# Optimization experiments

Hardware: AMD Instinct MI355X
Metric: run time of the kernel (lower is better)

## Reference

```python
import jax, jax.numpy as jnp
import numpy as np

N, E, F, H, C, ED = 10000, 160000, 4, 32, 4, 2  # nodes, edges, in_feat, hidden, classes, edge_dim


def _init(key, shape, fan_in):
    return jax.random.normal(key, shape, jnp.float32) / np.float32(np.sqrt(fan_in))


def setup_inputs() -> dict:
    key = jax.random.key(0)
    ks = iter(jax.random.split(key, 40))
    inp = {
        "x": jax.random.normal(next(ks), (N, F), jnp.float32),
        "edge_index": jax.random.randint(next(ks), (2, E), 0, N, dtype=jnp.int32),
        "edge_attr": jax.random.normal(next(ks), (E, ED), jnp.float32),
    }
    for i, din in enumerate([F, H, H]):
        inp[f"w1_{i}"] = _init(next(ks), (ED, H), ED)
        inp[f"b1_{i}"] = jnp.zeros((H,), jnp.float32)
        inp[f"w2_{i}"] = _init(next(ks), (H, din * H), H)
        inp[f"b2_{i}"] = jnp.zeros((din * H,), jnp.float32)
        inp[f"root_{i}"] = _init(next(ks), (din, H), din)
        inp[f"bias_{i}"] = jnp.zeros((H,), jnp.float32)
    inp["fc_w"] = _init(next(ks), (H, C), H)
    inp["fc_b"] = jnp.zeros((C,), jnp.float32)
    return inp


def _nnconv(x, src, dst, edge_attr, w1, b1, w2, b2, root, bias):
    # edge MLP -> per-edge weight matrix [E, din, H]
    h = jax.nn.relu(edge_attr @ w1 + b1)                      # [E, H]
    W = (h @ w2 + b2).reshape(E, x.shape[1], -1)              # [E, din, H]
    msg = jnp.einsum('ei,eio->eo', x[src], W)                 # gather + per-edge matvec
    agg = jax.ops.segment_sum(msg, dst, num_segments=N)       # scatter-add to targets
    return agg + x @ root + bias                              # root weight + bias (NNConv)


def reference(x, edge_index, edge_attr,
              w1_0, b1_0, w2_0, b2_0, root_0, bias_0,
              w1_1, b1_1, w2_1, b2_1, root_1, bias_1,
              w1_2, b1_2, w2_2, b2_2, root_2, bias_2,
              fc_w, fc_b):
    src, dst = edge_index[0], edge_index[1]
    layers = [(w1_0, b1_0, w2_0, b2_0, root_0, bias_0),
              (w1_1, b1_1, w2_1, b2_1, root_1, bias_1),
              (w1_2, b1_2, w2_2, b2_2, root_2, bias_2)]
    for p in layers:
        x = jax.nn.relu(_nnconv(x, src, dst, edge_attr, *p))  # dropout=0 -> no-op
    logits = x @ fc_w + fc_b
    return jax.nn.log_softmax(logits, axis=1)
```

## Files before the change

### kernel.cpp

```cpp
#include <hip/hip_runtime.h>
#include <hip/hip_bf16.h>
#include <math.h>

#define N_NODES 10000
#define N_EDGES 160000

typedef __attribute__((ext_vector_type(8))) short bf16x8;
typedef __attribute__((ext_vector_type(4))) float f32x4;

static __device__ inline unsigned short f2b(float v) {
    __hip_bfloat16 b = __float2bfloat16(v);
    return *reinterpret_cast<unsigned short*>(&b);
}

__global__ __launch_bounds__(256) void k_tw2z(const float* __restrict__ s0,
                                              const float* __restrict__ s1,
                                              const float* __restrict__ s2,
                                              float* __restrict__ t0,
                                              float* __restrict__ t1,
                                              float* __restrict__ t2,
                                              int* __restrict__ cnt) {
    int tid = blockIdx.x * 256 + threadIdx.x;
    if (tid < 10240) { cnt[tid] = 0; return; }
    int d = tid - 10240;
    if (d < 4096) {
        int i = d >> 10, j = d & 1023, o = j >> 5, k = j & 31;
        t0[d] = s0[k * 128 + i * 32 + o];
    } else if (d < 4096 + 32768) {
        int q = d - 4096;
        int i = q >> 10, j = q & 1023, o = j >> 5, k = j & 31;
        t1[q] = s1[k * 1024 + i * 32 + o];
    } else if (d < 4096 + 65536) {
        int q = d - 4096 - 32768;
        int i = q >> 10, j = q & 1023, o = j >> 5, k = j & 31;
        t2[q] = s2[k * 1024 + i * 32 + o];
    }
}

__global__ __launch_bounds__(256) void k_hist(const int* __restrict__ ei,
                                              int* __restrict__ cnt) {
    int e = blockIdx.x * 256 + threadIdx.x;
    if (e < N_EDGES) atomicAdd(&cnt[ei[e]], 1);
}

__global__ __launch_bounds__(256) void k_scan(const int* __restrict__ cnt,
                                              int* __restrict__ off,
                                              int* __restrict__ cursor) {
    __shared__ int part[256];
    int t = threadIdx.x;
    int base = t * 40;
    int s = 0;
    for (int i = 0; i < 40; ++i) {
        int idx = base + i;
        if (idx < N_NODES) s += cnt[idx];
    }
    part[t] = s;
    __syncthreads();
    for (int d = 1; d < 256; d <<= 1) {
        int v = (t >= d) ? part[t - d] : 0;
        __syncthreads();
        part[t] += v;
        __syncthreads();
    }
    int run = part[t] - s;
    for (int i = 0; i < 40; ++i) {
        int idx = base + i;
        if (idx < N_NODES) {
            off[idx] = run;
            cursor[idx] = run;
            run += cnt[idx];
        }
    }
    if (t == 255) off[N_NODES] = run;
}

__global__ __launch_bounds__(256) void k_scatter_h(const int* __restrict__ ei,
                                                   const float* __restrict__ ea,
                                                   int* __restrict__ cursor,
                                                   int* __restrict__ dst_s,
                                                   const float* __restrict__ w1a, const float* __restrict__ b1a,
                                                   const float* __restrict__ w1b, const float* __restrict__ b1b,
                                                   const float* __restrict__ w1c, const float* __restrict__ b1c,
                                                   unsigned short* __restrict__ h0,
                                                   unsigned short* __restrict__ h1,
                                                   unsigned short* __restrict__ h2) {
    int e = blockIdx.x * 256 + threadIdx.x;
    if (e >= N_EDGES) return;
    float a0 = ea[2 * e], a1 = ea[2 * e + 1];
    int src = ei[e], dst = ei[N_EDGES + e];
    int pos = atomicAdd(&cursor[src], 1);
    dst_s[pos] = dst;
    const float* W1[3] = {w1a, w1b, w1c};
    const float* B1[3] = {b1a, b1b, b1c};
    unsigned short* H[3] = {h0, h1, h2};
#pragma unroll
    for (int l = 0; l < 3; ++l) {
        unsigned int pk[16];
#pragma unroll
        for (int j = 0; j < 16; ++j) {
            float v0 = fmaxf(a0 * W1[l][2 * j]     + a1 * W1[l][32 + 2 * j]     + B1[l][2 * j],     0.f);
            float v1 = fmaxf(a0 * W1[l][2 * j + 1] + a1 * W1[l][32 + 2 * j + 1] + B1[l][2 * j + 1], 0.f);
            pk[j] = (unsigned int)f2b(v0) | ((unsigned int)f2b(v1) << 16);
        }
        uint4* dp = (uint4*)(H[l] + (size_t)pos * 32);
        dp[0] = make_uint4(pk[0], pk[1], pk[2], pk[3]);
        dp[1] = make_uint4(pk[4], pk[5], pk[6], pk[7]);
        dp[2] = make_uint4(pk[8], pk[9], pk[10], pk[11]);
        dp[3] = make_uint4(pk[12], pk[13], pk[14], pk[15]);
    }
}

template <int DIN, bool FIRST>
__global__ __launch_bounds__(256) void k_G(const float* __restrict__ xin,
                                           const float* __restrict__ w2t,
                                           const float* __restrict__ b2,
                                           const float* __restrict__ root,
                                           const float* __restrict__ bias,
                                           unsigned short* __restrict__ Gb,
                                           float* __restrict__ xb2,
                                           float* __restrict__ agg) {
    const int t = threadIdx.x;
    const int n0 = blockIdx.x * 16;

    __shared__ float xs[16 * DIN];
    for (int idx = t; idx < 16 * DIN; idx += 256) {
        int m = idx / DIN, i = idx - m * DIN;
        float v = xin[(size_t)(n0 + m) * DIN + i];
        if (!FIRST) v = v > 0.f ? v : 0.f;
        xs[idx] = v;
    }
    __syncthreads();

    float acc[16][4];
#pragma unroll
    for (int m = 0; m < 16; ++m)
        acc[m][0] = acc[m][1] = acc[m][2] = acc[m][3] = 0.f;

#pragma unroll
    for (int i = 0; i < DIN; ++i) {
        const float4 w = *(const float4*)(w2t + i * 1024 + t * 4);
#pragma unroll
        for (int m = 0; m < 16; ++m) {
            float xv = xs[m * DIN + i];
            acc[m][0] += xv * w.x;
            acc[m][1] += xv * w.y;
            acc[m][2] += xv * w.z;
            acc[m][3] += xv * w.w;
        }
    }
#pragma unroll
    for (int m = 0; m < 16; ++m) {
        unsigned int p0 = (unsigned int)f2b(acc[m][0]) | ((unsigned int)f2b(acc[m][1]) << 16);
        unsigned int p1 = (unsigned int)f2b(acc[m][2]) | ((unsigned int)f2b(acc[m][3]) << 16);
        *(uint2*)(Gb + (size_t)(n0 + m) * 1024 + t * 4) = make_uint2(p0, p1);
    }

    for (int idx = t; idx < 512; idx += 256) {
        int m = idx >> 5, o = idx & 31;
        float ab = 0.f, ar = bias[o];
#pragma unroll
        for (int i = 0; i < DIN; ++i) {
            float xv = xs[m * DIN + i];
            ab += xv * b2[i * 32 + o];
            ar += xv * root[i * 32 + o];
        }
        size_t p = (size_t)(n0 + m) * 32 + o;
        xb2[p] = ab;
        agg[p] = ar;
    }
}

__global__ __launch_bounds__(256) void k_edge(const int* __restrict__ off,
                                              const int* __restrict__ dst_s,
                                              const unsigned short* __restrict__ hb,
                                              const unsigned short* __restrict__ Gb,
                                              const float* __restrict__ xb2,
                                              float* __restrict__ agg) {
    int t = threadIdx.x;
    int lane = t & 63;
    int n = blockIdx.x * 4 + (t >> 6);
    int col = lane & 15;
    int quad = lane >> 4;

    const bf16x8 b_lo = *(const bf16x8*)(Gb + (size_t)n * 1024 + col * 32 + quad * 8);
    const bf16x8 b_hi = *(const bf16x8*)(Gb + (size_t)n * 1024 + (col + 16) * 32 + quad * 8);
    float xb_lo = xb2[(size_t)n * 32 + col];
    float xb_hi = xb2[(size_t)n * 32 + 16 + col];

    int jb = off[n], je = off[n + 1];
    for (int e0 = jb; e0 < je; e0 += 16) {
        int eA = e0 + col;
        bf16x8 afrag = {0, 0, 0, 0, 0, 0, 0, 0};
        if (eA < je) afrag = *(const bf16x8*)(hb + (size_t)eA * 32 + quad * 8);
        f32x4 acc_lo = {xb_lo, xb_lo, xb_lo, xb_lo};
        f32x4 acc_hi = {xb_hi, xb_hi, xb_hi, xb_hi};
        acc_lo = __builtin_amdgcn_mfma_f32_16x16x32_bf16(afrag, b_lo, acc_lo, 0, 0, 0);
        acc_hi = __builtin_amdgcn_mfma_f32_16x16x32_bf16(afrag, b_hi, acc_hi, 0, 0, 0);
#pragma unroll
        for (int r = 0; r < 4; ++r) {
            int er = e0 + quad * 4 + r;
            if (er < je) {
                int d = dst_s[er];
                atomicAdd(&agg[(size_t)d * 32 + col], acc_lo[r]);
                atomicAdd(&agg[(size_t)d * 32 + 16 + col], acc_hi[r]);
            }
        }
    }
}

__global__ __launch_bounds__(64) void k_final(const float* __restrict__ agg,
                                              const float* __restrict__ fcw,
                                              const float* __restrict__ fcb,
                                              float* __restrict__ out) {
    int n = blockIdx.x * 64 + threadIdx.x;
    if (n >= N_NODES) return;
    float l0 = fcb[0], l1 = fcb[1], l2 = fcb[2], l3 = fcb[3];
#pragma unroll
    for (int o = 0; o < 32; ++o) {
        float xv = agg[(size_t)n * 32 + o];
        xv = xv > 0.f ? xv : 0.f;
        l0 += xv * fcw[o * 4 + 0];
        l1 += xv * fcw[o * 4 + 1];
        l2 += xv * fcw[o * 4 + 2];
        l3 += xv * fcw[o * 4 + 3];
    }
    float m = fmaxf(fmaxf(l0, l1), fmaxf(l2, l3));
    float s = expf(l0 - m) + expf(l1 - m) + expf(l2 - m) + expf(l3 - m);
    float lse = m + logf(s);
    out[(size_t)n * 4 + 0] = l0 - lse;
    out[(size_t)n * 4 + 1] = l1 - lse;
    out[(size_t)n * 4 + 2] = l2 - lse;
    out[(size_t)n * 4 + 3] = l3 - lse;
}

extern "C" void kernel_launch(void* const* d_in, const int* in_sizes, int n_in,
                              void* d_out, int out_size, void* d_ws, size_t ws_size,
                              hipStream_t stream) {
    const float* x0 = (const float*)d_in[0];
    const int*   ei = (const int*)d_in[1];
    const float* ea = (const float*)d_in[2];
    const float *W1[3], *B1[3], *W2[3], *B2[3], *RT[3], *BS[3];
    for (int l = 0; l < 3; ++l) {
        W1[l] = (const float*)d_in[3 + 6 * l];
        B1[l] = (const float*)d_in[4 + 6 * l];
        W2[l] = (const float*)d_in[5 + 6 * l];
        B2[l] = (const float*)d_in[6 + 6 * l];
        RT[l] = (const float*)d_in[7 + 6 * l];
        BS[l] = (const float*)d_in[8 + 6 * l];
    }
    const float* fcw = (const float*)d_in[21];
    const float* fcb = (const float*)d_in[22];
    float* out = (float*)d_out;

    int*   cnt    = (int*)d_ws;
    int*   cursor = cnt + 10240;
    int*   off    = cursor + 10240;
    int*   dst_s  = off + 10240;
    float* w2t0   = (float*)(dst_s + 160000);
    float* w2t1   = w2t0 + 4096;
    float* w2t2   = w2t1 + 32768;
    float* xb2    = w2t2 + 32768;
    float* aggA   = xb2 + 320000;
    float* aggB   = aggA + 320000;
    unsigned short* h0 = (unsigned short*)(aggB + 320000);
    unsigned short* h1 = h0 + 5120000;
    unsigned short* h2 = h1 + 5120000;
    unsigned short* Gb = h2 + 5120000;

    const int gE256 = (N_EDGES + 255) / 256;
    const int gG    = N_NODES / 16;
    const int gEdge = N_NODES / 4;

    k_tw2z<<<312, 256, 0, stream>>>(W2[0], W2[1], W2[2], w2t0, w2t1, w2t2, cnt);
    k_hist<<<gE256, 256, 0, stream>>>(ei, cnt);
    k_scan<<<1, 256, 0, stream>>>(cnt, off, cursor);
    k_scatter_h<<<gE256, 256, 0, stream>>>(ei, ea, cursor, dst_s,
                                           W1[0], B1[0], W1[1], B1[1], W1[2], B1[2],
                                           h0, h1, h2);

    k_G<4, true><<<gG, 256, 0, stream>>>(x0, w2t0, B2[0], RT[0], BS[0], Gb, xb2, aggA);
    k_edge<<<gEdge, 256, 0, stream>>>(off, dst_s, h0, Gb, xb2, aggA);

    k_G<32, false><<<gG, 256, 0, stream>>>(aggA, w2t1, B2[1], RT[1], BS[1], Gb, xb2, aggB);
    k_edge<<<gEdge, 256, 0, stream>>>(off, dst_s, h1, Gb, xb2, aggB);

    k_G<32, false><<<gG, 256, 0, stream>>>(aggB, w2t2, B2[2], RT[2], BS[2], Gb, xb2, aggA);
    k_edge<<<gEdge, 256, 0, stream>>>(off, dst_s, h2, Gb, xb2, aggA);

    k_final<<<(N_NODES + 63) / 64, 64, 0, stream>>>(aggA, fcw, fcb, out);
}
```

Before: 278.4 us.

## Replace atomic scatter-add with dst-sorted message buffer and gather-reduce

Builds a second CSR keyed by destination node, with a per-edge slot map. Edge kernels now write each message to its slot in a dst-sorted buffer instead of doing float atomicAdds. The next layer's k_G and the final kernel sum each node's incoming messages before applying ReLU. This removes contended global float atomics but adds an extra histogram, scan, atomic cursor and a 20 MB message buffer that is written and read once per layer.

```diff
diff --git a/kernel.cpp b/kernel.cpp
--- a/kernel.cpp
+++ b/kernel.cpp
@@ -19,10 +19,10 @@
                                               float* __restrict__ t0,
                                               float* __restrict__ t1,
                                               float* __restrict__ t2,
-                                              int* __restrict__ cnt) {
+                                              int* __restrict__ cntz) {
     int tid = blockIdx.x * 256 + threadIdx.x;
-    if (tid < 10240) { cnt[tid] = 0; return; }
-    int d = tid - 10240;
+    if (tid < 20480) { cntz[tid] = 0; return; }
+    int d = tid - 20480;
     if (d < 4096) {
         int i = d >> 10, j = d & 1023, o = j >> 5, k = j & 31;
         t0[d] = s0[k * 128 + i * 32 + o];
@@ -37,22 +37,32 @@
     }
 }
 
-__global__ __launch_bounds__(256) void k_hist(const int* __restrict__ ei,
-                                              int* __restrict__ cnt) {
+__global__ __launch_bounds__(256) void k_hist2(const int* __restrict__ ei,
+                                               int* __restrict__ cnt,
+                                               int* __restrict__ cntd) {
     int e = blockIdx.x * 256 + threadIdx.x;
-    if (e < N_EDGES) atomicAdd(&cnt[ei[e]], 1);
-}
-
-__global__ __launch_bounds__(256) void k_scan(const int* __restrict__ cnt,
-                                              int* __restrict__ off,
-                                              int* __restrict__ cursor) {
+    if (e < N_EDGES) {
+        atomicAdd(&cnt[ei[e]], 1);
+        atomicAdd(&cntd[ei[N_EDGES + e]], 1);
+    }
+}
+
+__global__ __launch_bounds__(256) void k_scan2(const int* __restrict__ cnt,
+                                               const int* __restrict__ cntd,
+                                               int* __restrict__ off,
+                                               int* __restrict__ dst_off,
+                                               int* __restrict__ cursor,
+                                               int* __restrict__ cursord) {
+    const int* c; int* o; int* cu;
+    if (blockIdx.x == 0) { c = cnt;  o = off;     cu = cursor;  }
+    else                 { c = cntd; o = dst_off; cu = cursord; }
     __shared__ int part[256];
     int t = threadIdx.x;
     int base = t * 40;
     int s = 0;
     for (int i = 0; i < 40; ++i) {
         int idx = base + i;
-        if (idx < N_NODES) s += cnt[idx];
+        if (idx < N_NODES) s += c[idx];
     }
     part[t] = s;
     __syncthreads();
@@ -66,18 +76,19 @@
     for (int i = 0; i < 40; ++i) {
         int idx = base + i;
         if (idx < N_NODES) {
-            off[idx] = run;
-            cursor[idx] = run;
-            run += cnt[idx];
-        }
-    }
-    if (t == 255) off[N_NODES] = run;
+            o[idx] = run;
+            cu[idx] = run;
+            run += c[idx];
+        }
+    }
+    if (t == 255) o[N_NODES] = run;
 }
 
 __global__ __launch_bounds__(256) void k_scatter_h(const int* __restrict__ ei,
                                                    const float* __restrict__ ea,
                                                    int* __restrict__ cursor,
-                                                   int* __restrict__ dst_s,
+                                                   int* __restrict__ cursord,
+                                                   int* __restrict__ qmap,
                                                    const float* __restrict__ w1a, const float* __restrict__ b1a,
                                                    const float* __restrict__ w1b, const float* __restrict__ b1b,
                                                    const float* __restrict__ w1c, const float* __restrict__ b1c,
@@ -89,7 +100,8 @@
     float a0 = ea[2 * e], a1 = ea[2 * e + 1];
     int src = ei[e], dst = ei[N_EDGES + e];
     int pos = atomicAdd(&cursor[src], 1);
-    dst_s[pos] = dst;
+    int q   = atomicAdd(&cursord[dst], 1);
+    qmap[pos] = q;
     const float* W1[3] = {w1a, w1b, w1c};
     const float* B1[3] = {b1a, b1b, b1c};
     unsigned short* H[3] = {h0, h1, h2};
@@ -112,6 +124,8 @@
 
 template <int DIN, bool FIRST>
 __global__ __launch_bounds__(256) void k_G(const float* __restrict__ xin,
+                                           const int* __restrict__ dst_off,
+                                           const float* __restrict__ msgd,
                                            const float* __restrict__ w2t,
                                            const float* __restrict__ b2,
                                            const float* __restrict__ root,
@@ -123,11 +137,27 @@
     const int n0 = blockIdx.x * 16;
 
     __shared__ float xs[16 * DIN];
-    for (int idx = t; idx < 16 * DIN; idx += 256) {
-        int m = idx / DIN, i = idx - m * DIN;
-        float v = xin[(size_t)(n0 + m) * DIN + i];
-        if (!FIRST) v = v > 0.f ? v : 0.f;
-        xs[idx] = v;
+    if (FIRST) {
+        for (int idx = t; idx < 16 * DIN; idx += 256) {
+            int m = idx / DIN, i = idx - m * DIN;
+            xs[idx] = xin[(size_t)(n0 + m) * DIN + i];
+        }
+    } else {
+        for (int idx = t; idx < 512; idx += 256) {
+            int m = idx >> 5, i = idx & 31;
+            int n = n0 + m;
+            float v = xin[(size_t)n * 32 + i];
+            int jb = dst_off[n], je = dst_off[n + 1];
+            float v0 = 0.f, v1 = 0.f;
+            int j = jb;
+            for (; j + 1 < je; j += 2) {
+                v0 += msgd[(size_t)j * 32 + i];
+                v1 += msgd[(size_t)(j + 1) * 32 + i];
+            }
+            if (j < je) v0 += msgd[(size_t)j * 32 + i];
+            v += v0 + v1;
+            xs[idx] = v > 0.f ? v : 0.f;
+        }
     }
     __syncthreads();
 
@@ -171,11 +201,11 @@
 }
 
 __global__ __launch_bounds__(256) void k_edge(const int* __restrict__ off,
-                                              const int* __restrict__ dst_s,
+                                              const int* __restrict__ qmap,
                                               const unsigned short* __restrict__ hb,
                                               const unsigned short* __restrict__ Gb,
                                               const float* __restrict__ xb2,
-                                              float* __restrict__ agg) {
+                                              float* __restrict__ msgd) {
     int t = threadIdx.x;
     int lane = t & 63;
     int n = blockIdx.x * 4 + (t >> 6);
@@ -200,37 +230,55 @@
         for (int r = 0; r < 4; ++r) {
             int er = e0 + quad * 4 + r;
             if (er < je) {
-                int d = dst_s[er];
-                atomicAdd(&agg[(size_t)d * 32 + col], acc_lo[r]);
-                atomicAdd(&agg[(size_t)d * 32 + 16 + col], acc_hi[r]);
+                int q = qmap[er];
+                msgd[(size_t)q * 32 + col] = acc_lo[r];
+                msgd[(size_t)q * 32 + 16 + col] = acc_hi[r];
             }
         }
     }
 }
 
-__global__ __launch_bounds__(64) void k_final(const float* __restrict__ agg,
-                                              const float* __restrict__ fcw,
-                                              const float* __restrict__ fcb,
-                                              float* __restrict__ out) {
-    int n = blockIdx.x * 64 + threadIdx.x;
-    if (n >= N_NODES) return;
-    float l0 = fcb[0], l1 = fcb[1], l2 = fcb[2], l3 = fcb[3];
-#pragma unroll
-    for (int o = 0; o < 32; ++o) {
-        float xv = agg[(size_t)n * 32 + o];
-        xv = xv > 0.f ? xv : 0.f;
-        l0 += xv * fcw[o * 4 + 0];
-        l1 += xv * fcw[o * 4 + 1];
-        l2 += xv * fcw[o * 4 + 2];
-        l3 += xv * fcw[o * 4 + 3];
-    }
-    float m = fmaxf(fmaxf(l0, l1), fmaxf(l2, l3));
-    float s = expf(l0 - m) + expf(l1 - m) + expf(l2 - m) + expf(l3 - m);
-    float lse = m + logf(s);
-    out[(size_t)n * 4 + 0] = l0 - lse;
-    out[(size_t)n * 4 + 1] = l1 - lse;
-    out[(size_t)n * 4 + 2] = l2 - lse;
-    out[(size_t)n * 4 + 3] = l3 - lse;
+__global__ __launch_bounds__(256) void k_final(const float* __restrict__ agg,
+                                               const int* __restrict__ dst_off,
+                                               const float* __restrict__ msgd,
+                                               const float* __restrict__ fcw,
+                                               const float* __restrict__ fcb,
+                                               float* __restrict__ out) {
+    __shared__ float xs[8 * 32];
+    int t = threadIdx.x;
+    int m = t >> 5, o = t & 31;
+    int n = blockIdx.x * 8 + m;
+    float v = agg[(size_t)n * 32 + o];
+    int jb = dst_off[n], je = dst_off[n + 1];
+    float v0 = 0.f, v1 = 0.f;
+    int j = jb;
+    for (; j + 1 < je; j += 2) {
+        v0 += msgd[(size_t)j * 32 + o];
+        v1 += msgd[(size_t)(j + 1) * 32 + o];
+    }
+    if (j < je) v0 += msgd[(size_t)j * 32 + o];
+    v += v0 + v1;
+    xs[t] = v > 0.f ? v : 0.f;
+    __syncthreads();
+    if (t < 8) {
+        int nn = blockIdx.x * 8 + t;
+        float l0 = fcb[0], l1 = fcb[1], l2 = fcb[2], l3 = fcb[3];
+#pragma unroll
+        for (int oo = 0; oo < 32; ++oo) {
+            float xv = xs[t * 32 + oo];
+            l0 += xv * fcw[oo * 4 + 0];
+            l1 += xv * fcw[oo * 4 + 1];
+            l2 += xv * fcw[oo * 4 + 2];
+            l3 += xv * fcw[oo * 4 + 3];
+        }
+        float mx = fmaxf(fmaxf(l0, l1), fmaxf(l2, l3));
+        float s = expf(l0 - mx) + expf(l1 - mx) + expf(l2 - mx) + expf(l3 - mx);
+        float lse = mx + logf(s);
+        out[(size_t)nn * 4 + 0] = l0 - lse;
+        out[(size_t)nn * 4 + 1] = l1 - lse;
+        out[(size_t)nn * 4 + 2] = l2 - lse;
+        out[(size_t)nn * 4 + 3] = l3 - lse;
+    }
 }
 
 extern "C" void kernel_launch(void* const* d_in, const int* in_sizes, int n_in,
@@ -252,17 +300,21 @@
     const float* fcb = (const float*)d_in[22];
     float* out = (float*)d_out;
 
-    int*   cnt    = (int*)d_ws;
-    int*   cursor = cnt + 10240;
-    int*   off    = cursor + 10240;
-    int*   dst_s  = off + 10240;
-    float* w2t0   = (float*)(dst_s + 160000);
-    float* w2t1   = w2t0 + 4096;
-    float* w2t2   = w2t1 + 32768;
-    float* xb2    = w2t2 + 32768;
-    float* aggA   = xb2 + 320000;
-    float* aggB   = aggA + 320000;
-    unsigned short* h0 = (unsigned short*)(aggB + 320000);
+    int*   cnt     = (int*)d_ws;
+    int*   cntd    = cnt + 10240;
+    int*   cursor  = cntd + 10240;
+    int*   cursord = cursor + 10240;
+    int*   off     = cursord + 10240;
+    int*   dst_off = off + 10240;
+    int*   qmap    = dst_off + 10240;
+    float* w2t0    = (float*)(qmap + 160000);
+    float* w2t1    = w2t0 + 4096;
+    float* w2t2    = w2t1 + 32768;
+    float* xb2     = w2t2 + 32768;
+    float* aggA    = xb2 + 320000;
+    float* aggB    = aggA + 320000;
+    float* msgd    = aggB + 320000;
+    unsigned short* h0 = (unsigned short*)(msgd + 5120000);
     unsigned short* h1 = h0 + 5120000;
     unsigned short* h2 = h1 + 5120000;
     unsigned short* Gb = h2 + 5120000;
@@ -271,21 +323,21 @@
     const int gG    = N_NODES / 16;
     const int gEdge = N_NODES / 4;
 
-    k_tw2z<<<312, 256, 0, stream>>>(W2[0], W2[1], W2[2], w2t0, w2t1, w2t2, cnt);
-    k_hist<<<gE256, 256, 0, stream>>>(ei, cnt);
-    k_scan<<<1, 256, 0, stream>>>(cnt, off, cursor);
-    k_scatter_h<<<gE256, 256, 0, stream>>>(ei, ea, cursor, dst_s,
+    k_tw2z<<<352, 256, 0, stream>>>(W2[0], W2[1], W2[2], w2t0, w2t1, w2t2, cnt);
+    k_hist2<<<gE256, 256, 0, stream>>>(ei, cnt, cntd);
+    k_scan2<<<2, 256, 0, stream>>>(cnt, cntd, off, dst_off, cursor, cursord);
+    k_scatter_h<<<gE256, 256, 0, stream>>>(ei, ea, cursor, cursord, qmap,
                                            W1[0], B1[0], W1[1], B1[1], W1[2], B1[2],
                                            h0, h1, h2);
 
-    k_G<4, true><<<gG, 256, 0, stream>>>(x0, w2t0, B2[0], RT[0], BS[0], Gb, xb2, aggA);
-    k_edge<<<gEdge, 256, 0, stream>>>(off, dst_s, h0, Gb, xb2, aggA);
-
-    k_G<32, false><<<gG, 256, 0, stream>>>(aggA, w2t1, B2[1], RT[1], BS[1], Gb, xb2, aggB);
-    k_edge<<<gEdge, 256, 0, stream>>>(off, dst_s, h1, Gb, xb2, aggB);
-
-    k_G<32, false><<<gG, 256, 0, stream>>>(aggB, w2t2, B2[2], RT[2], BS[2], Gb, xb2, aggA);
-    k_edge<<<gEdge, 256, 0, stream>>>(off, dst_s, h2, Gb, xb2, aggA);
-
-    k_final<<<(N_NODES + 63) / 64, 64, 0, stream>>>(aggA, fcw, fcb, out);
-}
+    k_G<4, true><<<gG, 256, 0, stream>>>(x0, dst_off, msgd, w2t0, B2[0], RT[0], BS[0], Gb, xb2, aggA);
+    k_edge<<<gEdge, 256, 0, stream>>>(off, qmap, h0, Gb, xb2, msgd);
+
+    k_G<32, false><<<gG, 256, 0, stream>>>(aggA, dst_off, msgd, w2t1, B2[1], RT[1], BS[1], Gb, xb2, aggB);
+    k_edge<<<gEdge, 256, 0, stream>>>(off, qmap, h1, Gb, xb2, msgd);
+
+    k_G<32, false><<<gG, 256, 0, stream>>>(aggB, dst_off, msgd, w2t2, B2[2], RT[2], BS[2], Gb, xb2, aggA);
+    k_edge<<<gEdge, 256, 0, stream>>>(off, qmap, h2, Gb, xb2, msgd);
+
+    k_final<<<(N_NODES + 7) / 8, 256, 0, stream>>>(aggA, dst_off, msgd, fcw, fcb, out);
+}
```

Measured after the change: 281.4 us. About the same (+1.1%).
